# Kernel optimization log

Measured on AMD Instinct MI355X. Metric: run time of the kernel, lower is better.

The kernel has to match this reference:

```python
import jax, jax.numpy as jnp
import numpy as np

TOPK = 2
GATE_THRESHOLD = 0.5
GATE_ALPHA = 0.1
EPS = 1e-8


def setup_inputs() -> dict:
    key = jax.random.key(0)
    x = jax.random.normal(key, (8192, 1024), dtype=jnp.float32)
    return {"x": x}


def reference(x):
    B, D = x.shape
    # F.normalize(p=2, eps): x / max(||x||, eps)
    norm = jnp.linalg.norm(x, axis=-1, keepdims=True)
    xn = x / jnp.maximum(norm, EPS)

    # pairwise dots; diagonal (self) masked to -1; NN search is no_grad
    dots = jax.lax.stop_gradient(xn @ xn.T)  # [B, B]
    diag = jnp.arange(B)
    dots = dots.at[diag, diag].set(-1.0)
    _, idx = jax.lax.top_k(dots, TOPK)  # [B, TOPK]

    nn_vecs = xn[idx]  # [B, TOPK, D]
    # torch PairwiseDistance(2, eps): ||x1 - x2 + eps||_2
    diff = xn[:, None, :] - nn_vecs + EPS
    distances = jnp.sqrt(jnp.sum(diff * diff, axis=-1)).reshape(-1)  # [B*TOPK]
    losses = -jnp.log(distances + EPS)

    # gate enabled since gate_threshold > 0
    alpha = max(GATE_ALPHA, 1e-6)
    gate = jax.nn.sigmoid((losses - GATE_THRESHOLD) / alpha)
    lg = losses * gate
    weighted_mean = lg.mean()
    gated_mean = lg.sum() / jnp.maximum(gate.sum(), 1.0)
    return 0.5 * weighted_mean + 0.5 * gated_mean
```

## Files before the change

kernel.cpp:

```cpp
#include <hip/hip_runtime.h>
#include <math.h>

#define NROWS 8192
#define DIM   1024
#define NCHUNK 64
#define NTRI  2080

typedef __bf16 bf16x8 __attribute__((ext_vector_type(8)));
typedef float  f32x4  __attribute__((ext_vector_type(4)));

__device__ __forceinline__ unsigned short f2bf(float f) {
    unsigned int u = __float_as_uint(f);
    u = (u + 0x7FFFu + ((u >> 16) & 1u)) >> 16;
    return (unsigned short)u;
}

__device__ __forceinline__ void gld16(const void* g, void* l) {
    __builtin_amdgcn_global_load_lds(
        (__attribute__((address_space(1))) void*)g,
        (__attribute__((address_space(3))) void*)l,
        16, 0, 0);
}

__device__ __forceinline__ void t2push(float& a1, float& a2, float v) {
    float hi = fmaxf(a1, v);
    float lo = fminf(a1, v);
    a1 = hi;
    a2 = fmaxf(a2, lo);
}

__device__ __forceinline__ void t2merge(float& a1, float& a2, float b1, float b2) {
    float hi = fmaxf(a1, b1);
    float lo = fminf(a1, b1);
    a1 = hi;
    a2 = fmaxf(fmaxf(a2, b2), lo);
}

__global__ __launch_bounds__(256) void knorm(const float* __restrict__ x,
                                             unsigned short* __restrict__ xn) {
    const int row = blockIdx.x;
    const int t = threadIdx.x;
    const float4 v = ((const float4*)(x + (size_t)row * DIM))[t];
    float ss = v.x * v.x + v.y * v.y + v.z * v.z + v.w * v.w;
    #pragma unroll
    for (int d = 1; d < 64; d <<= 1) ss += __shfl_xor(ss, d);
    __shared__ float wsum[4];
    if ((t & 63) == 0) wsum[t >> 6] = ss;
    __syncthreads();
    const float tot = wsum[0] + wsum[1] + wsum[2] + wsum[3];
    const float inv = 1.0f / fmaxf(sqrtf(tot), 1e-8f);
    uint2 o;
    o.x = (unsigned)f2bf(v.x * inv) | ((unsigned)f2bf(v.y * inv) << 16);
    o.y = (unsigned)f2bf(v.z * inv) | ((unsigned)f2bf(v.w * inv) << 16);
    *(uint2*)(xn + (size_t)row * DIM + t * 4) = o;
}

__global__ __launch_bounds__(256) void kgram(const unsigned short* __restrict__ xn,
                                             float2* __restrict__ top2) {
    const int bid = blockIdx.x;
    int by = (int)((sqrtf(8.0f * (float)bid + 1.0f) - 1.0f) * 0.5f);
    while ((by + 1) * (by + 2) / 2 <= bid) by++;
    while (by * (by + 1) / 2 > bid) by--;
    const int bx = bid - by * (by + 1) / 2;

    const int t = threadIdx.x;
    const int w = t >> 6, lane = t & 63;
    const int wr = w >> 1, wc = w & 1;
    const int g = lane >> 4, c = lane & 15;

    __shared__ __align__(16) unsigned short As[128 * 32];
    __shared__ __align__(16) unsigned short Bs[128 * 32];
    __shared__ float st2r[2][128][2];
    __shared__ float st2c[2][128][2];

    f32x4 acc[4][4];
    #pragma unroll
    for (int m = 0; m < 4; m++)
        #pragma unroll
        for (int n = 0; n < 4; n++) acc[m][n] = (f32x4)0.0f;

    const int rA0 = t >> 2, cp0 = (t & 3) * 8;
    const unsigned short* gA0 = xn + (size_t)(by * 128 + rA0) * DIM + cp0;
    const unsigned short* gA1 = gA0 + (size_t)64 * DIM;
    const unsigned short* gB0 = xn + (size_t)(bx * 128 + rA0) * DIM + cp0;
    const unsigned short* gB1 = gB0 + (size_t)64 * DIM;
    char* lA0 = (char*)As + (size_t)w * 1024;
    char* lA1 = (char*)As + 4096 + (size_t)w * 1024;
    char* lB0 = (char*)Bs + (size_t)w * 1024;
    char* lB1 = (char*)Bs + 4096 + (size_t)w * 1024;

    for (int kk = 0; kk < DIM; kk += 32) {
        __syncthreads();
        gld16(gA0 + kk, lA0);
        gld16(gA1 + kk, lA1);
        gld16(gB0 + kk, lB0);
        gld16(gB1 + kk, lB1);
        __syncthreads();

        bf16x8 af[4], bf[4];
        #pragma unroll
        for (int m = 0; m < 4; m++)
            af[m] = *(const bf16x8*)(As + (wr * 64 + m * 16 + c) * 32 + g * 8);
        #pragma unroll
        for (int n = 0; n < 4; n++)
            bf[n] = *(const bf16x8*)(Bs + (wc * 64 + n * 16 + c) * 32 + g * 8);
        #pragma unroll
        for (int m = 0; m < 4; m++)
            #pragma unroll
            for (int n = 0; n < 4; n++)
                acc[m][n] = __builtin_amdgcn_mfma_f32_16x16x32_bf16(af[m], bf[n], acc[m][n], 0, 0, 0);
    }

    const bool diagTile = (bx == by);

    #pragma unroll
    for (int m = 0; m < 4; m++) {
        #pragma unroll
        for (int r = 0; r < 4; r++) {
            const int lrow = wr * 64 + m * 16 + g * 4 + r;
            float a1 = -1e30f, a2 = -1e30f;
            #pragma unroll
            for (int n = 0; n < 4; n++) {
                float v = acc[m][n][r];
                if (diagTile && (wc * 64 + n * 16 + c) == lrow) v = -2.0f;
                t2push(a1, a2, v);
            }
            #pragma unroll
            for (int d = 1; d < 16; d <<= 1) {
                float b1 = __shfl_xor(a1, d);
                float b2 = __shfl_xor(a2, d);
                t2merge(a1, a2, b1, b2);
            }
            if (c == 0) { st2r[wc][lrow][0] = a1; st2r[wc][lrow][1] = a2; }
        }
    }

    if (!diagTile) {
        #pragma unroll
        for (int n = 0; n < 4; n++) {
            const int lcol = wc * 64 + n * 16 + c;
            float a1 = -1e30f, a2 = -1e30f;
            #pragma unroll
            for (int m = 0; m < 4; m++)
                #pragma unroll
                for (int r = 0; r < 4; r++)
                    t2push(a1, a2, acc[m][n][r]);
            #pragma unroll
            for (int d = 16; d < 64; d <<= 1) {
                float b1 = __shfl_xor(a1, d);
                float b2 = __shfl_xor(a2, d);
                t2merge(a1, a2, b1, b2);
            }
            if (g == 0) { st2c[wr][lcol][0] = a1; st2c[wr][lcol][1] = a2; }
        }
    }

    __syncthreads();
    if (t < 128) {
        float a1 = st2r[0][t][0], a2 = st2r[0][t][1];
        t2merge(a1, a2, st2r[1][t][0], st2r[1][t][1]);
        top2[(size_t)(by * 128 + t) * NCHUNK + bx] = make_float2(a1, a2);
    }
    if (!diagTile && t < 128) {
        float a1 = st2c[0][t][0], a2 = st2c[0][t][1];
        t2merge(a1, a2, st2c[1][t][0], st2c[1][t][1]);
        top2[(size_t)(bx * 128 + t) * NCHUNK + by] = make_float2(a1, a2);
    }
}

__global__ __launch_bounds__(256) void kloss(const float2* __restrict__ top2,
                                             float2* __restrict__ partials) {
    const int t = threadIdx.x;
    const int w = t >> 6, lane = t & 63;
    const int row = blockIdx.x * 4 + w;
    float2 q = top2[(size_t)row * NCHUNK + lane];
    float a1 = q.x, a2 = q.y;
    #pragma unroll
    for (int d = 1; d < 64; d <<= 1) {
        float b1 = __shfl_xor(a1, d);
        float b2 = __shfl_xor(a2, d);
        t2merge(a1, a2, b1, b2);
    }
    __shared__ float2 wsum[4];
    if (lane == 0) {
        float slg = 0.0f, sg = 0.0f;
        float vs[2] = {a1, a2};
        #pragma unroll
        for (int i = 0; i < 2; i++) {
            float dd = sqrtf(fmaxf(2.0f - 2.0f * vs[i], 0.0f));
            float loss = -logf(dd + 1e-8f);
            float gate = 1.0f / (1.0f + expf(-(loss - 0.5f) * 10.0f));
            slg += loss * gate;
            sg += gate;
        }
        wsum[w] = make_float2(slg, sg);
    }
    __syncthreads();
    if (t == 0) {
        float a = 0.0f, b = 0.0f;
        #pragma unroll
        for (int i = 0; i < 4; i++) { a += wsum[i].x; b += wsum[i].y; }
        partials[blockIdx.x] = make_float2(a, b);
    }
}

__global__ __launch_bounds__(256) void kfinal(const float2* __restrict__ partials,
                                              float* __restrict__ out) {
    const int t = threadIdx.x;
    float a = 0.0f, b = 0.0f;
    for (int i = t; i < 2048; i += 256) {
        float2 p = partials[i];
        a += p.x; b += p.y;
    }
    #pragma unroll
    for (int d = 1; d < 64; d <<= 1) {
        a += __shfl_xor(a, d);
        b += __shfl_xor(b, d);
    }
    __shared__ float2 ws4[4];
    if ((t & 63) == 0) ws4[t >> 6] = make_float2(a, b);
    __syncthreads();
    if (t == 0) {
        float A = 0.0f, Bb = 0.0f;
        #pragma unroll
        for (int i = 0; i < 4; i++) { A += ws4[i].x; Bb += ws4[i].y; }
        float wm = A / 16384.0f;
        float gm = A / fmaxf(Bb, 1.0f);
        out[0] = 0.5f * wm + 0.5f * gm;
    }
}

extern "C" void kernel_launch(void* const* d_in, const int* in_sizes, int n_in,
                              void* d_out, int out_size, void* d_ws, size_t ws_size,
                              hipStream_t stream) {
    const float* x = (const float*)d_in[0];
    unsigned short* xn = (unsigned short*)d_ws;
    float2* top2 = (float2*)((char*)d_ws + (size_t)16 * 1024 * 1024);
    float2* partials = (float2*)((char*)d_ws + (size_t)20 * 1024 * 1024);
    float* out = (float*)d_out;

    knorm<<<NROWS, 256, 0, stream>>>(x, xn);
    kgram<<<NTRI, 256, 0, stream>>>(xn, top2);
    kloss<<<2048, 256, 0, stream>>>(top2, partials);
    kfinal<<<1, 256, 0, stream>>>(partials, out);
}
```

Measured before the change: 180.8 us.

## Double-buffer gram K-loop, remap tile order, use DPP row reductions, per-wave norm

```diff
diff --git a/kernel.cpp b/kernel.cpp
--- a/kernel.cpp
+++ b/kernel.cpp
@@ -22,6 +22,12 @@
         16, 0, 0);
 }
 
+template<int N>
+__device__ __forceinline__ float dppror(float v) {
+    return __int_as_float(__builtin_amdgcn_update_dpp(
+        0, __float_as_int(v), 0x120 + N, 0xF, 0xF, false));
+}
+
 __device__ __forceinline__ void t2push(float& a1, float& a2, float v) {
     float hi = fmaxf(a1, v);
     float lo = fminf(a1, v);
@@ -38,26 +44,33 @@
 
 __global__ __launch_bounds__(256) void knorm(const float* __restrict__ x,
                                              unsigned short* __restrict__ xn) {
-    const int row = blockIdx.x;
-    const int t = threadIdx.x;
-    const float4 v = ((const float4*)(x + (size_t)row * DIM))[t];
-    float ss = v.x * v.x + v.y * v.y + v.z * v.z + v.w * v.w;
+    const int w = threadIdx.x >> 6, lane = threadIdx.x & 63;
+    const int row = blockIdx.x * 4 + w;
+    const float4* src = (const float4*)(x + (size_t)row * DIM);
+    float4 v[4];
+    float ss = 0.0f;
+    #pragma unroll
+    for (int i = 0; i < 4; i++) {
+        v[i] = src[lane + 64 * i];
+        ss += v[i].x * v[i].x + v[i].y * v[i].y + v[i].z * v[i].z + v[i].w * v[i].w;
+    }
     #pragma unroll
     for (int d = 1; d < 64; d <<= 1) ss += __shfl_xor(ss, d);
-    __shared__ float wsum[4];
-    if ((t & 63) == 0) wsum[t >> 6] = ss;
-    __syncthreads();
-    const float tot = wsum[0] + wsum[1] + wsum[2] + wsum[3];
-    const float inv = 1.0f / fmaxf(sqrtf(tot), 1e-8f);
-    uint2 o;
-    o.x = (unsigned)f2bf(v.x * inv) | ((unsigned)f2bf(v.y * inv) << 16);
-    o.y = (unsigned)f2bf(v.z * inv) | ((unsigned)f2bf(v.w * inv) << 16);
-    *(uint2*)(xn + (size_t)row * DIM + t * 4) = o;
+    const float inv = 1.0f / fmaxf(sqrtf(ss), 1e-8f);
+    unsigned short* dst = xn + (size_t)row * DIM;
+    #pragma unroll
+    for (int i = 0; i < 4; i++) {
+        uint2 o;
+        o.x = (unsigned)f2bf(v[i].x * inv) | ((unsigned)f2bf(v[i].y * inv) << 16);
+        o.y = (unsigned)f2bf(v[i].z * inv) | ((unsigned)f2bf(v[i].w * inv) << 16);
+        *(uint2*)(dst + (size_t)(lane + 64 * i) * 4) = o;
+    }
 }
 
 __global__ __launch_bounds__(256) void kgram(const unsigned short* __restrict__ xn,
                                              float2* __restrict__ top2) {
-    const int bid = blockIdx.x;
+    const int bid0 = blockIdx.x;
+    const int bid = (bid0 & 7) * (NTRI / 8) + (bid0 >> 3);
     int by = (int)((sqrtf(8.0f * (float)bid + 1.0f) - 1.0f) * 0.5f);
     while ((by + 1) * (by + 2) / 2 <= bid) by++;
     while (by * (by + 1) / 2 > bid) by--;
@@ -68,8 +81,8 @@
     const int wr = w >> 1, wc = w & 1;
     const int g = lane >> 4, c = lane & 15;
 
-    __shared__ __align__(16) unsigned short As[128 * 32];
-    __shared__ __align__(16) unsigned short Bs[128 * 32];
+    __shared__ __align__(16) unsigned short As[2][128 * 32];
+    __shared__ __align__(16) unsigned short Bs[2][128 * 32];
     __shared__ float st2r[2][128][2];
     __shared__ float st2c[2][128][2];
 
@@ -84,31 +97,37 @@
     const unsigned short* gA1 = gA0 + (size_t)64 * DIM;
     const unsigned short* gB0 = xn + (size_t)(bx * 128 + rA0) * DIM + cp0;
     const unsigned short* gB1 = gB0 + (size_t)64 * DIM;
-    char* lA0 = (char*)As + (size_t)w * 1024;
-    char* lA1 = (char*)As + 4096 + (size_t)w * 1024;
-    char* lB0 = (char*)Bs + (size_t)w * 1024;
-    char* lB1 = (char*)Bs + 4096 + (size_t)w * 1024;
-
+
+    auto STAGE = [&](int buf, int kk) {
+        gld16(gA0 + kk, (char*)&As[buf][0] + (size_t)w * 1024);
+        gld16(gA1 + kk, (char*)&As[buf][0] + 4096 + (size_t)w * 1024);
+        gld16(gB0 + kk, (char*)&Bs[buf][0] + (size_t)w * 1024);
+        gld16(gB1 + kk, (char*)&Bs[buf][0] + 4096 + (size_t)w * 1024);
+    };
+
+    STAGE(0, 0);
+    __syncthreads();
+
+    int cur = 0;
+    #pragma unroll 2
     for (int kk = 0; kk < DIM; kk += 32) {
-        __syncthreads();
-        gld16(gA0 + kk, lA0);
-        gld16(gA1 + kk, lA1);
-        gld16(gB0 + kk, lB0);
-        gld16(gB1 + kk, lB1);
-        __syncthreads();
+        if (kk + 32 < DIM) STAGE(cur ^ 1, kk + 32);
 
         bf16x8 af[4], bf[4];
         #pragma unroll
         for (int m = 0; m < 4; m++)
-            af[m] = *(const bf16x8*)(As + (wr * 64 + m * 16 + c) * 32 + g * 8);
+            af[m] = *(const bf16x8*)(&As[cur][0] + (wr * 64 + m * 16 + c) * 32 + g * 8);
         #pragma unroll
         for (int n = 0; n < 4; n++)
-            bf[n] = *(const bf16x8*)(Bs + (wc * 64 + n * 16 + c) * 32 + g * 8);
+            bf[n] = *(const bf16x8*)(&Bs[cur][0] + (wc * 64 + n * 16 + c) * 32 + g * 8);
         #pragma unroll
         for (int m = 0; m < 4; m++)
             #pragma unroll
             for (int n = 0; n < 4; n++)
                 acc[m][n] = __builtin_amdgcn_mfma_f32_16x16x32_bf16(af[m], bf[n], acc[m][n], 0, 0, 0);
+
+        __syncthreads();
+        cur ^= 1;
     }
 
     const bool diagTile = (bx == by);
@@ -125,12 +144,10 @@
                 if (diagTile && (wc * 64 + n * 16 + c) == lrow) v = -2.0f;
                 t2push(a1, a2, v);
             }
-            #pragma unroll
-            for (int d = 1; d < 16; d <<= 1) {
-                float b1 = __shfl_xor(a1, d);
-                float b2 = __shfl_xor(a2, d);
-                t2merge(a1, a2, b1, b2);
-            }
+            { float b1 = dppror<1>(a1), b2 = dppror<1>(a2); t2merge(a1, a2, b1, b2); }
+            { float b1 = dppror<2>(a1), b2 = dppror<2>(a2); t2merge(a1, a2, b1, b2); }
+            { float b1 = dppror<4>(a1), b2 = dppror<4>(a2); t2merge(a1, a2, b1, b2); }
+            { float b1 = dppror<8>(a1), b2 = dppror<8>(a2); t2merge(a1, a2, b1, b2); }
             if (c == 0) { st2r[wc][lrow][0] = a1; st2r[wc][lrow][1] = a2; }
         }
     }
@@ -239,7 +256,7 @@
     float2* partials = (float2*)((char*)d_ws + (size_t)20 * 1024 * 1024);
     float* out = (float*)d_out;
 
-    knorm<<<NROWS, 256, 0, stream>>>(x, xn);
+    knorm<<<NROWS / 4, 256, 0, stream>>>(x, xn);
     kgram<<<NTRI, 256, 0, stream>>>(xn, top2);
     kloss<<<2048, 256, 0, stream>>>(top2, partials);
     kfinal<<<1, 256, 0, stream>>>(partials, out);
```

After: 176.3 us. -2.5%, faster.
